# Performance work log

Measured on AMD Instinct MI355X. Metric: run time of the kernel, lower is better.

Reference implementation:

```python
import jax, jax.numpy as jnp
import numpy as np

D_MODEL = 1024
NUM_HEADS = 16
HEAD_SIZE = D_MODEL // NUM_HEADS
ROPE_BASE = 10000.0
RMS_EPS = 1e-6


def rms_norm(x, scale):
    # torchtune RMSNorm: fp32 compute, eps=1e-6, learned scale
    xf = x.astype(jnp.float32)
    n = xf * jax.lax.rsqrt(jnp.mean(xf * xf, axis=-1, keepdims=True) + RMS_EPS)
    return (n * scale).astype(x.dtype)


def rope(x):
    # torchtune RotaryPositionalEmbeddings: interleaved pairs. x: [B,T,H,hd]
    B, T, H, hd = x.shape
    half = hd // 2
    theta = 1.0 / (ROPE_BASE ** (jnp.arange(0, hd, 2, dtype=jnp.float32) / hd))  # [half]
    ang = jnp.arange(T, dtype=jnp.float32)[:, None] * theta[None, :]  # [T,half]
    cos = jnp.cos(ang)[None, :, None, :]  # [1,T,1,half]
    sin = jnp.sin(ang)[None, :, None, :]
    xs = x.reshape(B, T, H, half, 2)
    x0, x1 = xs[..., 0], xs[..., 1]
    out = jnp.stack([x0 * cos - x1 * sin, x1 * cos + x0 * sin], axis=-1)
    return out.reshape(B, T, H, hd).astype(x.dtype)


def setup_inputs() -> dict:
    key = jax.random.key(0)
    ks = jax.random.split(key, 10)
    s = 0.02
    D = D_MODEL
    return {
        "x": jax.random.normal(ks[0], (2, 2048, D), dtype=jnp.float32),
        "rms_scale": jnp.ones((D,), dtype=jnp.float32),
        "in_proj_w": jax.random.normal(ks[1], (3 * D, D), dtype=jnp.float32) * s,
        "in_proj_b": jnp.zeros((3 * D,), dtype=jnp.float32),
        "out_proj_w": jax.random.normal(ks[2], (D, D), dtype=jnp.float32) * s,
        "out_proj_b": jnp.zeros((D,), dtype=jnp.float32),
        "w1": jax.random.normal(ks[3], (4 * D, D), dtype=jnp.float32) * s,
        "b1": jnp.zeros((4 * D,), dtype=jnp.float32),
        "w2": jax.random.normal(ks[4], (D, 4 * D), dtype=jnp.float32) * s,
        "b2": jnp.zeros((D,), dtype=jnp.float32),
    }


def reference(x, rms_scale, in_proj_w, in_proj_b, out_proj_w, out_proj_b, w1, b1, w2, b2):
    B, T, D = x.shape
    H, hd = NUM_HEADS, HEAD_SIZE

    xn = rms_norm(x, rms_scale)
    # RoPE on pre-projection q/k (as in original module), value = xn
    q_in = rope(xn.reshape(B, T, H, hd)).reshape(B, T, D)
    k_in = rope(xn.reshape(B, T, H, hd)).reshape(B, T, D)
    v_in = xn

    Wq, Wk, Wv = jnp.split(in_proj_w, 3, axis=0)
    bq, bk, bv = jnp.split(in_proj_b, 3, axis=0)
    q = (q_in @ Wq.T + bq).reshape(B, T, H, hd).transpose(0, 2, 1, 3)  # [B,H,T,hd]
    k = (k_in @ Wk.T + bk).reshape(B, T, H, hd).transpose(0, 2, 1, 3)
    v = (v_in @ Wv.T + bv).reshape(B, T, H, hd).transpose(0, 2, 1, 3)

    scores = jnp.einsum('bhqd,bhkd->bhqk', q, k) / jnp.sqrt(jnp.float32(hd))
    causal = jnp.tril(jnp.ones((T, T), dtype=bool))  # True = keep
    scores = jnp.where(causal[None, None], scores, jnp.float32(-1e30))
    attn = jax.nn.softmax(scores, axis=-1)
    ctx = jnp.einsum('bhqk,bhkd->bhqd', attn, v)  # [B,H,T,hd]
    attn_out = ctx.transpose(0, 2, 1, 3).reshape(B, T, D) @ out_proj_w.T + out_proj_b

    # NOTE: original overwrites x with attention output (no residual on attention)
    y = attn_out
    yn = rms_norm(y, rms_scale)
    ffn = jax.nn.silu(yn @ w1.T + b1) @ w2.T + b2
    return y + ffn
```

## Files before the change

### kernel.cpp

```cpp
#include <hip/hip_runtime.h>
#include <math.h>
#include <stdint.h>

#define D_MODEL 1024
#define NUM_HEADS 16
#define HEAD_SIZE 64
#define SEQ_T 2048

typedef __bf16 bf16;
typedef __bf16 bf16x8 __attribute__((ext_vector_type(8)));
typedef float f32x4 __attribute__((ext_vector_type(4)));

__device__ __forceinline__ void gld_lds16(const bf16* g, bf16* l) {
    __builtin_amdgcn_global_load_lds(
        (__attribute__((address_space(1))) void*)(const_cast<bf16*>(g)),
        (__attribute__((address_space(3))) void*)(l), 16, 0, 0);
}

struct __align__(8) b4pack { bf16 v[4]; };

__global__ __launch_bounds__(256) void cast_all_weights(const float* __restrict__ s0, bf16* __restrict__ d0, int n0,
                                                        const float* __restrict__ s1, bf16* __restrict__ d1, int n1,
                                                        const float* __restrict__ s2, bf16* __restrict__ d2, int n2,
                                                        const float* __restrict__ s3, bf16* __restrict__ d3, int n3) {
    int i = (blockIdx.x * 256 + threadIdx.x) * 4;
    const float* src;
    bf16* dst;
    if (i < n0) { src = s0; dst = d0; }
    else if (i < n0 + n1) { i -= n0; src = s1; dst = d1; }
    else if (i < n0 + n1 + n2) { i -= n0 + n1; src = s2; dst = d2; }
    else { i -= n0 + n1 + n2; if (i >= n3) return; src = s3; dst = d3; }
    float4 v = *(const float4*)(src + i);
    b4pack o;
    o.v[0] = (bf16)v.x; o.v[1] = (bf16)v.y; o.v[2] = (bf16)v.z; o.v[3] = (bf16)v.w;
    *(b4pack*)(dst + i) = o;
}

__global__ __launch_bounds__(256) void rmsnorm_rope_kernel(const float* __restrict__ x,
                                                           const float* __restrict__ scale,
                                                           bf16* __restrict__ xn,
                                                           bf16* __restrict__ rp, int T) {
    __shared__ float red[4];
    int row = blockIdx.x;
    int t = row % T;
    const float* xp = x + (size_t)row * D_MODEL;
    int tid = threadIdx.x;
    float4 xv = *(const float4*)(xp + tid * 4);
    float s = xv.x * xv.x + xv.y * xv.y + xv.z * xv.z + xv.w * xv.w;
    for (int off = 32; off; off >>= 1) s += __shfl_down(s, off);
    if ((tid & 63) == 0) red[tid >> 6] = s;
    __syncthreads();
    if (tid == 0) red[0] = red[0] + red[1] + red[2] + red[3];
    __syncthreads();
    float inv = rsqrtf(red[0] * (1.0f / D_MODEL) + 1e-6f);
    float4 sc = *(const float4*)(scale + tid * 4);
    float n0 = xv.x * inv * sc.x, n1 = xv.y * inv * sc.y;
    float n2 = xv.z * inv * sc.z, n3 = xv.w * inv * sc.w;
    b4pack pn;
    pn.v[0] = (bf16)n0; pn.v[1] = (bf16)n1; pn.v[2] = (bf16)n2; pn.v[3] = (bf16)n3;
    *(b4pack*)(xn + (size_t)row * D_MODEL + tid * 4) = pn;
    int p0 = 2 * tid;
    float th0 = expf(-0.2878231366242557f * (float)(p0 & 31));
    float th1 = expf(-0.2878231366242557f * (float)((p0 + 1) & 31));
    float s0, c0, s1, c1;
    sincosf((float)t * th0, &s0, &c0);
    sincosf((float)t * th1, &s1, &c1);
    b4pack pr;
    pr.v[0] = (bf16)(n0 * c0 - n1 * s0);
    pr.v[1] = (bf16)(n1 * c0 + n0 * s0);
    pr.v[2] = (bf16)(n2 * c1 - n3 * s1);
    pr.v[3] = (bf16)(n3 * c1 + n2 * s1);
    *(b4pack*)(rp + (size_t)row * D_MODEL + tid * 4) = pr;
}

__global__ __launch_bounds__(256) void rmsnorm_kernel(const float* __restrict__ x,
                                                      const float* __restrict__ scale,
                                                      bf16* __restrict__ out) {
    __shared__ float red[4];
    int row = blockIdx.x;
    const float* xp = x + (size_t)row * D_MODEL;
    bf16* op = out + (size_t)row * D_MODEL;
    int tid = threadIdx.x;
    float s = 0.f;
    for (int i = tid; i < D_MODEL; i += 256) { float v = xp[i]; s += v * v; }
    for (int off = 32; off; off >>= 1) s += __shfl_down(s, off);
    if ((tid & 63) == 0) red[tid >> 6] = s;
    __syncthreads();
    if (tid == 0) red[0] = red[0] + red[1] + red[2] + red[3];
    __syncthreads();
    float inv = rsqrtf(red[0] * (1.0f / D_MODEL) + 1e-6f);
    for (int i = tid; i < D_MODEL; i += 256) op[i] = (bf16)(xp[i] * inv * scale[i]);
}

template <int ACT, int ADD, int OUT_BF16, int VT>
__global__ __launch_bounds__(256) void gemm_bf16(const bf16* __restrict__ A,
                                                 const bf16* __restrict__ A2, int splitN,
                                                 const bf16* __restrict__ W,
                                                 const float* __restrict__ bias,
                                                 float* __restrict__ Cf,
                                                 bf16* __restrict__ Cb,
                                                 bf16* __restrict__ Vtp, int Tlen,
                                                 int M, int N, int K) {
    __shared__ __align__(16) bf16 As[2][128 * 64];
    __shared__ __align__(16) bf16 Bs[2][128 * 64];
    int tid = threadIdx.x;
    int m0 = blockIdx.y * 128, n0 = blockIdx.x * 128;
    const bf16* Ag = (n0 < splitN) ? A : A2;

    int lane = tid & 63, w = tid >> 6;
    int wm = w >> 1, wn = w & 1;
    int lm = lane & 15, quad = lane >> 4;
    int lm7 = lm & 7;

    f32x4 acc[4][4];
#pragma unroll
    for (int i = 0; i < 4; i++)
#pragma unroll
        for (int j = 0; j < 4; j++)
#pragma unroll
            for (int r = 0; r < 4; r++) acc[i][j][r] = 0.f;

    int nt = K >> 6;

#pragma unroll
    for (int i = 0; i < 4; i++) {
        int cch = tid + 256 * i;
        int r = cch >> 3, cc = (cch & 7) ^ (r & 7);
        gld_lds16(Ag + (size_t)(m0 + r) * K + cc * 8, &As[0][0] + cch * 8);
        gld_lds16(W  + (size_t)(n0 + r) * K + cc * 8, &Bs[0][0] + cch * 8);
    }

    for (int t = 0; t < nt; ++t) {
        int cur = t & 1;
        if (t + 1 < nt) {
            int k0 = (t + 1) << 6;
            bf16* as = &As[cur ^ 1][0];
            bf16* bs = &Bs[cur ^ 1][0];
#pragma unroll
            for (int i = 0; i < 4; i++) {
                int cch = tid + 256 * i;
                int r = cch >> 3, cc = (cch & 7) ^ (r & 7);
                gld_lds16(Ag + (size_t)(m0 + r) * K + k0 + cc * 8, as + cch * 8);
                gld_lds16(W  + (size_t)(n0 + r) * K + k0 + cc * 8, bs + cch * 8);
            }
            asm volatile("s_waitcnt vmcnt(8)" ::: "memory");
        } else {
            asm volatile("s_waitcnt vmcnt(0)" ::: "memory");
        }
        __builtin_amdgcn_s_barrier();

        const bf16* as = &As[cur][0];
        const bf16* bs = &Bs[cur][0];
        bf16x8 af[4][2], bfr[4][2];
#pragma unroll
        for (int i = 0; i < 4; i++) {
            int row = wm * 64 + i * 16 + lm;
#pragma unroll
            for (int h2 = 0; h2 < 2; h2++)
                af[i][h2] = *(const bf16x8*)&as[row * 64 + ((h2 * 4 + quad) ^ lm7) * 8];
        }
#pragma unroll
        for (int j = 0; j < 4; j++) {
            int row = wn * 64 + j * 16 + lm;
#pragma unroll
            for (int h2 = 0; h2 < 2; h2++)
                bfr[j][h2] = *(const bf16x8*)&bs[row * 64 + ((h2 * 4 + quad) ^ lm7) * 8];
        }
#pragma unroll
        for (int i = 0; i < 4; i++)
#pragma unroll
            for (int j = 0; j < 4; j++) {
                acc[i][j] = __builtin_amdgcn_mfma_f32_16x16x32_bf16(af[i][0], bfr[j][0], acc[i][j], 0, 0, 0);
                acc[i][j] = __builtin_amdgcn_mfma_f32_16x16x32_bf16(af[i][1], bfr[j][1], acc[i][j], 0, 0, 0);
            }
        asm volatile("" ::: "memory");
        __builtin_amdgcn_s_barrier();
    }

    if (VT && n0 >= 2 * D_MODEL) {
#pragma unroll
        for (int j = 0; j < 4; j++) {
            int col = n0 + wn * 64 + j * 16 + lm;
            int dimg = col - 2 * D_MODEL;
            float bv = bias[col];
#pragma unroll
            for (int i = 0; i < 4; i++) {
                int row0 = m0 + wm * 64 + i * 16 + quad * 4;
                int bb = row0 / Tlen, t0 = row0 % Tlen;
                b4pack pk;
#pragma unroll
                for (int r = 0; r < 4; r++) pk.v[r] = (bf16)(acc[i][j][r] + bv);
                *(b4pack*)(Vtp + ((size_t)bb * D_MODEL + dimg) * Tlen + t0) = pk;
            }
        }
        return;
    }

#pragma unroll
    for (int j = 0; j < 4; j++) {
        int col = n0 + wn * 64 + j * 16 + lm;
        float bv = bias[col];
#pragma unroll
        for (int i = 0; i < 4; i++) {
#pragma unroll
            for (int r = 0; r < 4; r++) {
                int row = m0 + wm * 64 + i * 16 + quad * 4 + r;
                float v = acc[i][j][r] + bv;
                if (ACT == 1) v = v / (1.f + __expf(-v));
                size_t idx = (size_t)row * N + col;
                if (ADD) v += Cf[idx];
                if (OUT_BF16) Cb[idx] = (bf16)v;
                else Cf[idx] = v;
            }
        }
    }
}

template <int ADD>
__global__ __launch_bounds__(256) void gemm_bf16_skinny2(const bf16* __restrict__ A,
                                                         const bf16* __restrict__ W,
                                                         const float* __restrict__ bias,
                                                         float* __restrict__ Cf,
                                                         int M, int N, int K) {
    __shared__ __align__(16) bf16 As[2][64 * 64];
    __shared__ __align__(16) bf16 Bs[2][128 * 64];
    int tid = threadIdx.x;

    int nblk = gridDim.x;
    int q = nblk >> 3;
    int swz = (blockIdx.x & 7) * q + (blockIdx.x >> 3);
    int nb = swz & 7;
    int mb = swz >> 3;
    int m0 = mb * 64, n0 = nb * 128;

    int lane = tid & 63, w = tid >> 6;
    int wm = w >> 1, wn = w & 1;
    int lm = lane & 15, quad = lane >> 4;
    int lm7 = lm & 7;

    int ar0 = tid >> 3, ac0 = (tid & 7) ^ (ar0 & 7);
    int t1 = tid + 256;
    int ar1 = t1 >> 3, ac1 = (t1 & 7) ^ (ar1 & 7);

    f32x4 acc[2][4];
#pragma unroll
    for (int i = 0; i < 2; i++)
#pragma unroll
        for (int j = 0; j < 4; j++)
#pragma unroll
            for (int r = 0; r < 4; r++) acc[i][j][r] = 0.f;

    int nt = K >> 6;

    {
        gld_lds16(A + (size_t)(m0 + ar0) * K + ac0 * 8, &As[0][0] + tid * 8);
        gld_lds16(A + (size_t)(m0 + ar1) * K + ac1 * 8, &As[0][0] + t1 * 8);
#pragma unroll
        for (int i = 0; i < 4; i++) {
            int c = tid + 256 * i;
            int r = c >> 3, cc = (c & 7) ^ (r & 7);
            gld_lds16(W + (size_t)(n0 + r) * K + cc * 8, &Bs[0][0] + c * 8);
        }
    }

    for (int t = 0; t < nt; ++t) {
        int cur = t & 1;
        if (t + 1 < nt) {
            int k0 = (t + 1) << 6;
            bf16* as = &As[cur ^ 1][0];
            bf16* bs = &Bs[cur ^ 1][0];
            gld_lds16(A + (size_t)(m0 + ar0) * K + k0 + ac0 * 8, as + tid * 8);
            gld_lds16(A + (size_t)(m0 + ar1) * K + k0 + ac1 * 8, as + t1 * 8);
#pragma unroll
            for (int i = 0; i < 4; i++) {
                int c = tid + 256 * i;
                int r = c >> 3, cc = (c & 7) ^ (r & 7);
                gld_lds16(W + (size_t)(n0 + r) * K + k0 + cc * 8, bs + c * 8);
            }
            asm volatile("s_waitcnt vmcnt(6)" ::: "memory");
        } else {
            asm volatile("s_waitcnt vmcnt(0)" ::: "memory");
        }
        __builtin_amdgcn_s_barrier();

        const bf16* as = &As[cur][0];
        const bf16* bs = &Bs[cur][0];
        bf16x8 af[2][2], bfr[4][2];
#pragma unroll
        for (int i = 0; i < 2; i++) {
            int row = wm * 32 + i * 16 + lm;
#pragma unroll
            for (int h = 0; h < 2; h++)
                af[i][h] = *(const bf16x8*)&as[row * 64 + ((h * 4 + quad) ^ lm7) * 8];
        }
#pragma unroll
        for (int j = 0; j < 4; j++) {
            int row = wn * 64 + j * 16 + lm;
#pragma unroll
            for (int h = 0; h < 2; h++)
                bfr[j][h] = *(const bf16x8*)&bs[row * 64 + ((h * 4 + quad) ^ lm7) * 8];
        }
#pragma unroll
        for (int i = 0; i < 2; i++)
#pragma unroll
            for (int j = 0; j < 4; j++) {
                acc[i][j] = __builtin_amdgcn_mfma_f32_16x16x32_bf16(af[i][0], bfr[j][0], acc[i][j], 0, 0, 0);
                acc[i][j] = __builtin_amdgcn_mfma_f32_16x16x32_bf16(af[i][1], bfr[j][1], acc[i][j], 0, 0, 0);
            }
        asm volatile("" ::: "memory");
        __builtin_amdgcn_s_barrier();
    }

#pragma unroll
    for (int j = 0; j < 4; j++) {
        int col = n0 + wn * 64 + j * 16 + lm;
        float bv = bias[col];
#pragma unroll
        for (int i = 0; i < 2; i++) {
#pragma unroll
            for (int r = 0; r < 4; r++) {
                int row = m0 + wm * 32 + i * 16 + quad * 4 + r;
                float v = acc[i][j][r] + bv;
                size_t idx = (size_t)row * N + col;
                if (ADD) v += Cf[idx];
                Cf[idx] = v;
            }
        }
    }
}

__global__ __launch_bounds__(256, 2) void attn_mfma_kernel(const bf16* __restrict__ QKV,
                                                           const bf16* __restrict__ Vt,
                                                           bf16* __restrict__ Og, int T) {
    __shared__ __align__(16) bf16 Ks[2][2][64 * 64];
    __shared__ __align__(16) bf16 Vs[2][2][64 * 64];
    __shared__ __align__(16) bf16 Ps[4 * 16 * 64];
    const int ldq = 3 * D_MODEL;
    int bidx = blockIdx.x;
    int c = bidx & 7;
    int rest = bidx >> 3;
    int p = rest & 15;
    int bhoct = rest >> 4;
    int bh = bhoct * 8 + c;
    int qtA = 31 - p, qtB = p;
    int h = bh & (NUM_HEADS - 1), b = bh / NUM_HEADS;
    int tid = threadIdx.x;
    int w = tid >> 6, lane = tid & 63;
    int lm = lane & 15, quad = lane >> 4;
    int qrowA = qtA * 64 + w * 16, qrowB = qtB * 64 + w * 16;

    int s0 = tid, s1 = tid + 256;
    int sr0 = s0 >> 3, sc0 = (s0 & 7) ^ (sr0 & 7);
    int sr1 = s1 >> 3, sc1 = (s1 & 7) ^ (sr1 & 7);

    const bf16* QpA = QKV + ((size_t)(b * T + qrowA + lm)) * ldq + h * HEAD_SIZE + quad * 8;
    bf16x8 qfA0 = *(const bf16x8*)QpA;
    bf16x8 qfA1 = *(const bf16x8*)(QpA + 32);
    const bf16* QpB = QKV + ((size_t)(b * T + qrowB + lm)) * ldq + h * HEAD_SIZE + quad * 8;
    bf16x8 qfB0 = *(const bf16x8*)QpB;
    bf16x8 qfB1 = *(const bf16x8*)(QpB + 32);

    const bf16* Kbase = QKV + ((size_t)b * T) * ldq + D_MODEL + h * HEAD_SIZE;
    const bf16* Vbase = Vt + ((size_t)b * D_MODEL + h * HEAD_SIZE) * T;
    const float C = 0.1803368801111204f;
    bf16* PsW = Ps + w * 16 * 64;
    int lm7 = lm & 7;

    bf16x8 ones;
#pragma unroll
    for (int i = 0; i < 8; i++) ones[i] = (bf16)1.0f;

    f32x4 oA[4], oB[4], laccA, laccB;
#pragma unroll
    for (int r = 0; r < 4; r++) {
        oA[r] = (f32x4){0.f, 0.f, 0.f, 0.f};
        oB[r] = (f32x4){0.f, 0.f, 0.f, 0.f};
        laccA[r] = 0.f; laccB[r] = 0.f;
    }

    int nktA = (qtA + 2) >> 1;
    int nktB = (qtB + 2) >> 1;

    auto stage = [&](int buf, int k0) {
        gld_lds16(Kbase + (size_t)(k0 + sr0) * ldq + sc0 * 8, &Ks[buf][0][0] + s0 * 8);
        gld_lds16(Kbase + (size_t)(k0 + sr1) * ldq + sc1 * 8, &Ks[buf][0][0] + s1 * 8);
        gld_lds16(Kbase + (size_t)(k0 + 64 + sr0) * ldq + sc0 * 8, &Ks[buf][1][0] + s0 * 8);
        gld_lds16(Kbase + (size_t)(k0 + 64 + sr1) * ldq + sc1 * 8, &Ks[buf][1][0] + s1 * 8);
        gld_lds16(Vbase + (size_t)sr0 * T + k0 + sc0 * 8, &Vs[buf][0][0] + s0 * 8);
        gld_lds16(Vbase + (size_t)sr1 * T + k0 + sc1 * 8, &Vs[buf][0][0] + s1 * 8);
        gld_lds16(Vbase + (size_t)sr0 * T + k0 + 64 + sc0 * 8, &Vs[buf][1][0] + s0 * 8);
        gld_lds16(Vbase + (size_t)sr1 * T + k0 + 64 + sc1 * 8, &Vs[buf][1][0] + s1 * 8);
    };

    auto run_tile = [&](int cur, int k0, bf16x8 qf0, bf16x8 qf1, int qrow0,
                        f32x4 (&o)[4], f32x4& lacc, bool lastmask) {
        f32x4 sa[2][4];
        __builtin_amdgcn_s_setprio(1);
#pragma unroll
        for (int u = 0; u < 2; u++) {
            const bf16* Ksu = &Ks[cur][u][0];
#pragma unroll
            for (int jb = 0; jb < 4; jb++) {
                int n = jb * 16 + lm;
                bf16x8 kf0 = *(const bf16x8*)&Ksu[(n * 8 + (quad ^ lm7)) * 8];
                bf16x8 kf1 = *(const bf16x8*)&Ksu[(n * 8 + ((quad + 4) ^ lm7)) * 8];
                f32x4 a = {0.f, 0.f, 0.f, 0.f};
                a = __builtin_amdgcn_mfma_f32_16x16x32_bf16(qf0, kf0, a, 0, 0, 0);
                a = __builtin_amdgcn_mfma_f32_16x16x32_bf16(qf1, kf1, a, 0, 0, 0);
                sa[u][jb] = a;
            }
        }
        __builtin_amdgcn_s_setprio(0);
        if (lastmask) {
#pragma unroll
            for (int u = 0; u < 2; u++)
#pragma unroll
                for (int jb = 0; jb < 4; jb++)
#pragma unroll
                    for (int r = 0; r < 4; r++)
                        if (k0 + u * 64 + jb * 16 + lm > qrow0 + quad * 4 + r)
                            sa[u][jb][r] = -3.0e38f;
        }
#pragma unroll
        for (int u = 0; u < 2; u++) {
            const bf16* Vsu = &Vs[cur][u][0];
#pragma unroll
            for (int jb = 0; jb < 4; jb++) {
                int g = jb * 2 + (lm >> 3);
#pragma unroll
                for (int r = 0; r < 4; r++) {
                    int row = quad * 4 + r;
                    float pv = exp2f(sa[u][jb][r] * C);
                    PsW[row * 64 + ((g ^ (row & 7)) * 8) + lm7] = (bf16)pv;
                }
            }
            bf16x8 pf0 = *(const bf16x8*)&PsW[lm * 64 + ((quad ^ lm7) * 8)];
            bf16x8 pf1 = *(const bf16x8*)&PsW[lm * 64 + (((quad + 4) ^ lm7) * 8)];
            __builtin_amdgcn_s_setprio(1);
#pragma unroll
            for (int db = 0; db < 4; db++) {
                int n = db * 16 + lm;
                bf16x8 vf0 = *(const bf16x8*)&Vsu[(n * 8 + (quad ^ lm7)) * 8];
                bf16x8 vf1 = *(const bf16x8*)&Vsu[(n * 8 + ((quad + 4) ^ lm7)) * 8];
                o[db] = __builtin_amdgcn_mfma_f32_16x16x32_bf16(pf0, vf0, o[db], 0, 0, 0);
                o[db] = __builtin_amdgcn_mfma_f32_16x16x32_bf16(pf1, vf1, o[db], 0, 0, 0);
            }
            lacc = __builtin_amdgcn_mfma_f32_16x16x32_bf16(pf0, ones, lacc, 0, 0, 0);
            lacc = __builtin_amdgcn_mfma_f32_16x16x32_bf16(pf1, ones, lacc, 0, 0, 0);
            __builtin_amdgcn_s_setprio(0);
        }
    };

    stage(0, 0);
    for (int kt = 0; kt < nktA; kt++) {
        int cur = kt & 1;
        if (kt + 1 < nktA) {
            stage(cur ^ 1, (kt + 1) * 128);
            asm volatile("s_waitcnt vmcnt(8)" ::: "memory");
        } else {
            asm volatile("s_waitcnt vmcnt(0)" ::: "memory");
        }
        __builtin_amdgcn_s_barrier();
        asm volatile("" ::: "memory");
        int k0 = kt * 128;
        run_tile(cur, k0, qfA0, qfA1, qrowA, oA, laccA, kt == nktA - 1);
        if (kt < nktB)
            run_tile(cur, k0, qfB0, qfB1, qrowB, oB, laccB, kt == nktB - 1);
        asm volatile("" ::: "memory");
        __builtin_amdgcn_s_barrier();
    }

    {
        float inv[4];
#pragma unroll
        for (int r = 0; r < 4; r++) inv[r] = 1.f / laccA[r];
        bf16* Ob = Og + ((size_t)(b * T + qrowA + quad * 4)) * D_MODEL + h * HEAD_SIZE + lm;
#pragma unroll
        for (int r = 0; r < 4; r++)
#pragma unroll
            for (int db = 0; db < 4; db++)
                Ob[(size_t)r * D_MODEL + db * 16] = (bf16)(oA[db][r] * inv[r]);
    }
    {
        float inv[4];
#pragma unroll
        for (int r = 0; r < 4; r++) inv[r] = 1.f / laccB[r];
        bf16* Ob = Og + ((size_t)(b * T + qrowB + quad * 4)) * D_MODEL + h * HEAD_SIZE + lm;
#pragma unroll
        for (int r = 0; r < 4; r++)
#pragma unroll
            for (int db = 0; db < 4; db++)
                Ob[(size_t)r * D_MODEL + db * 16] = (bf16)(oB[db][r] * inv[r]);
    }
}

extern "C" void kernel_launch(void* const* d_in, const int* in_sizes, int n_in,
                              void* d_out, int out_size, void* d_ws, size_t ws_size,
                              hipStream_t stream) {
    const float* x          = (const float*)d_in[0];
    const float* rms_scale  = (const float*)d_in[1];
    const float* in_proj_w  = (const float*)d_in[2];
    const float* in_proj_b  = (const float*)d_in[3];
    const float* out_proj_w = (const float*)d_in[4];
    const float* out_proj_b = (const float*)d_in[5];
    const float* w1         = (const float*)d_in[6];
    const float* b1         = (const float*)d_in[7];
    const float* w2         = (const float*)d_in[8];
    const float* b2         = (const float*)d_in[9];
    float* out = (float*)d_out;

    const int rows = in_sizes[0] / D_MODEL;
    const int T = SEQ_T;
    const int B = rows / T;
    const int D = D_MODEL;

    bf16* inwb  = (bf16*)d_ws;
    bf16* outwb = inwb + (size_t)3 * D * D;
    bf16* w1b   = outwb + (size_t)D * D;
    bf16* w2b   = w1b + (size_t)4 * D * D;
    bf16* XNb   = w2b + (size_t)4 * D * D;
    bf16* RPb   = XNb + (size_t)rows * D;
    bf16* QKV   = RPb + (size_t)rows * D;
    bf16* Vt    = QKV + (size_t)rows * 3 * D;
    bf16* CTXb  = XNb;
    bf16* YNb   = RPb;
    bf16* H1b   = QKV;

    {
        int n0 = 3 * D * D, n1 = D * D, n2 = 4 * D * D, n3 = 4 * D * D;
        int tot4 = (n0 + n1 + n2 + n3) / 4;
        cast_all_weights<<<(tot4 + 255) / 256, 256, 0, stream>>>(
            in_proj_w, inwb, n0, out_proj_w, outwb, n1, w1, w1b, n2, w2, w2b, n3);
    }
    rmsnorm_rope_kernel<<<rows, 256, 0, stream>>>(x, rms_scale, XNb, RPb, T);
    {
        dim3 g(3 * D / 128, rows / 128);
        gemm_bf16<0, 0, 1, 1><<<g, 256, 0, stream>>>(RPb, XNb, 2 * D, inwb, in_proj_b,
                                                     nullptr, QKV, Vt, T, rows, 3 * D, D);
    }
    attn_mfma_kernel<<<B * NUM_HEADS * (T / 128), 256, 0, stream>>>(QKV, Vt, CTXb, T);
    {
        int nblk = (D / 128) * (rows / 64);
        gemm_bf16_skinny2<0><<<nblk, 256, 0, stream>>>(CTXb, outwb, out_proj_b, out,
                                                       rows, D, D);
    }
    rmsnorm_kernel<<<rows, 256, 0, stream>>>(out, rms_scale, YNb);
    {
        dim3 g(4 * D / 128, rows / 128);
        gemm_bf16<1, 0, 1, 0><<<g, 256, 0, stream>>>(YNb, YNb, 4 * D, w1b, b1,
                                                     nullptr, H1b, nullptr, 1, rows, 4 * D, D);
    }
    {
        int nblk = (D / 128) * (rows / 64);
        gemm_bf16_skinny2<1><<<nblk, 256, 0, stream>>>(H1b, w2b, b2, out,
                                                       rows, D, 4 * D);
    }
}
```

Before: 332.8 us.

## Split-K the skinny output GEMMs with atomic accumulation and bias prefill

The two N=1024 GEMMs (out-projection and FFN down-projection) now split K in two and accumulate partial tiles into the fp32 output with atomic adds, which doubles the block count. The output buffer is pre-filled with the out-projection bias inside the weight-cast kernel, so the first GEMM adds only partial sums. The second GEMM adds b2 from its first split on top of the existing output. This is meant to raise occupancy on a grid that launched too few blocks for the CU count. In exchange it adds atomic traffic, an extra full write of the output, and a float summation order that is no longer deterministic.

```diff
diff --git a/kernel.cpp b/kernel.cpp
--- a/kernel.cpp
+++ b/kernel.cpp
@@ -22,14 +22,22 @@
 __global__ __launch_bounds__(256) void cast_all_weights(const float* __restrict__ s0, bf16* __restrict__ d0, int n0,
                                                         const float* __restrict__ s1, bf16* __restrict__ d1, int n1,
                                                         const float* __restrict__ s2, bf16* __restrict__ d2, int n2,
-                                                        const float* __restrict__ s3, bf16* __restrict__ d3, int n3) {
+                                                        const float* __restrict__ s3, bf16* __restrict__ d3, int n3,
+                                                        const float* __restrict__ bsrc, float* __restrict__ bdst, int n4) {
     int i = (blockIdx.x * 256 + threadIdx.x) * 4;
     const float* src;
     bf16* dst;
     if (i < n0) { src = s0; dst = d0; }
     else if (i < n0 + n1) { i -= n0; src = s1; dst = d1; }
     else if (i < n0 + n1 + n2) { i -= n0 + n1; src = s2; dst = d2; }
-    else { i -= n0 + n1 + n2; if (i >= n3) return; src = s3; dst = d3; }
+    else if (i < n0 + n1 + n2 + n3) { i -= n0 + n1 + n2; src = s3; dst = d3; }
+    else {
+        i -= n0 + n1 + n2 + n3;
+        if (i >= n4) return;
+        float4 b = *(const float4*)(bsrc + (i & (D_MODEL - 1)));
+        *(float4*)(bdst + i) = b;
+        return;
+    }
     float4 v = *(const float4*)(src + i);
     b4pack o;
     o.v[0] = (bf16)v.x; o.v[1] = (bf16)v.y; o.v[2] = (bf16)v.z; o.v[3] = (bf16)v.w;
@@ -216,12 +224,12 @@
     }
 }
 
-template <int ADD>
-__global__ __launch_bounds__(256) void gemm_bf16_skinny2(const bf16* __restrict__ A,
-                                                         const bf16* __restrict__ W,
-                                                         const float* __restrict__ bias,
-                                                         float* __restrict__ Cf,
-                                                         int M, int N, int K) {
+template <int BIAS0, int SPLIT>
+__global__ __launch_bounds__(256) void gemm_bf16_skinny_sk(const bf16* __restrict__ A,
+                                                           const bf16* __restrict__ W,
+                                                           const float* __restrict__ bias,
+                                                           float* __restrict__ Cf,
+                                                           int M, int N, int K) {
     __shared__ __align__(16) bf16 As[2][64 * 64];
     __shared__ __align__(16) bf16 Bs[2][128 * 64];
     int tid = threadIdx.x;
@@ -230,8 +238,13 @@
     int q = nblk >> 3;
     int swz = (blockIdx.x & 7) * q + (blockIdx.x >> 3);
     int nb = swz & 7;
-    int mb = swz >> 3;
+    int rem = swz >> 3;
+    int mblocks = M >> 6;
+    int mb = rem % mblocks;
+    int sp = rem / mblocks;
     int m0 = mb * 64, n0 = nb * 128;
+    int kc = K / SPLIT;
+    int kbeg = sp * kc;
 
     int lane = tid & 63, w = tid >> 6;
     int wm = w >> 1, wn = w & 1;
@@ -250,23 +263,23 @@
 #pragma unroll
             for (int r = 0; r < 4; r++) acc[i][j][r] = 0.f;
 
-    int nt = K >> 6;
-
-    {
-        gld_lds16(A + (size_t)(m0 + ar0) * K + ac0 * 8, &As[0][0] + tid * 8);
-        gld_lds16(A + (size_t)(m0 + ar1) * K + ac1 * 8, &As[0][0] + t1 * 8);
+    int nt = kc >> 6;
+
+    {
+        gld_lds16(A + (size_t)(m0 + ar0) * K + kbeg + ac0 * 8, &As[0][0] + tid * 8);
+        gld_lds16(A + (size_t)(m0 + ar1) * K + kbeg + ac1 * 8, &As[0][0] + t1 * 8);
 #pragma unroll
         for (int i = 0; i < 4; i++) {
             int c = tid + 256 * i;
             int r = c >> 3, cc = (c & 7) ^ (r & 7);
-            gld_lds16(W + (size_t)(n0 + r) * K + cc * 8, &Bs[0][0] + c * 8);
+            gld_lds16(W + (size_t)(n0 + r) * K + kbeg + cc * 8, &Bs[0][0] + c * 8);
         }
     }
 
     for (int t = 0; t < nt; ++t) {
         int cur = t & 1;
         if (t + 1 < nt) {
-            int k0 = (t + 1) << 6;
+            int k0 = kbeg + ((t + 1) << 6);
             bf16* as = &As[cur ^ 1][0];
             bf16* bs = &Bs[cur ^ 1][0];
             gld_lds16(A + (size_t)(m0 + ar0) * K + k0 + ac0 * 8, as + tid * 8);
@@ -314,16 +327,13 @@
 #pragma unroll
     for (int j = 0; j < 4; j++) {
         int col = n0 + wn * 64 + j * 16 + lm;
-        float bv = bias[col];
+        float bv = (BIAS0 && sp == 0) ? bias[col] : 0.f;
 #pragma unroll
         for (int i = 0; i < 2; i++) {
 #pragma unroll
             for (int r = 0; r < 4; r++) {
                 int row = m0 + wm * 32 + i * 16 + quad * 4 + r;
-                float v = acc[i][j][r] + bv;
-                size_t idx = (size_t)row * N + col;
-                if (ADD) v += Cf[idx];
-                Cf[idx] = v;
+                unsafeAtomicAdd(Cf + (size_t)row * N + col, acc[i][j][r] + bv);
             }
         }
     }
@@ -528,9 +538,11 @@
 
     {
         int n0 = 3 * D * D, n1 = D * D, n2 = 4 * D * D, n3 = 4 * D * D;
-        int tot4 = (n0 + n1 + n2 + n3) / 4;
+        int n4 = rows * D;
+        int tot4 = (n0 + n1 + n2 + n3 + n4) / 4;
         cast_all_weights<<<(tot4 + 255) / 256, 256, 0, stream>>>(
-            in_proj_w, inwb, n0, out_proj_w, outwb, n1, w1, w1b, n2, w2, w2b, n3);
+            in_proj_w, inwb, n0, out_proj_w, outwb, n1, w1, w1b, n2, w2, w2b, n3,
+            out_proj_b, out, n4);
     }
     rmsnorm_rope_kernel<<<rows, 256, 0, stream>>>(x, rms_scale, XNb, RPb, T);
     {
@@ -540,9 +552,9 @@
     }
     attn_mfma_kernel<<<B * NUM_HEADS * (T / 128), 256, 0, stream>>>(QKV, Vt, CTXb, T);
     {
-        int nblk = (D / 128) * (rows / 64);
-        gemm_bf16_skinny2<0><<<nblk, 256, 0, stream>>>(CTXb, outwb, out_proj_b, out,
-                                                       rows, D, D);
+        int nblk = 2 * (rows / 64) * (D / 128);
+        gemm_bf16_skinny_sk<0, 2><<<nblk, 256, 0, stream>>>(CTXb, outwb, out_proj_b,
+                                                            out, rows, D, D);
     }
     rmsnorm_kernel<<<rows, 256, 0, stream>>>(out, rms_scale, YNb);
     {
@@ -551,8 +563,8 @@
                                                      nullptr, H1b, nullptr, 1, rows, 4 * D, D);
     }
     {
-        int nblk = (D / 128) * (rows / 64);
-        gemm_bf16_skinny2<1><<<nblk, 256, 0, stream>>>(H1b, w2b, b2, out,
-                                                       rows, D, 4 * D);
-    }
-}
+        int nblk = 2 * (rows / 64) * (D / 128);
+        gemm_bf16_skinny_sk<1, 2><<<nblk, 256, 0, stream>>>(H1b, w2b, b2,
+                                                            out, rows, D, 4 * D);
+    }
+}
```

New measurement: 366.0 us. 10.0% more time.

## Use split-K 128x128 GEMM with atomic accumulation for FFN down-projection

Applied to the files above, without the earlier changes.

Replaces the 64x128-tile skinny kernel for the w2 GEMM (K=4096) with a 128x128-tile kernel that splits K in two and atomically adds partial results into the output, which already holds the attention output for the residual. Larger tiles raise data reuse per block, and split-K keeps the grid at 512 blocks. The cost is float atomic traffic to the output and a non-deterministic summation order.

```diff
diff --git a/kernel.cpp b/kernel.cpp
--- a/kernel.cpp
+++ b/kernel.cpp
@@ -216,6 +216,114 @@
     }
 }
 
+template <int SPLIT>
+__global__ __launch_bounds__(256) void gemm128_sk(const bf16* __restrict__ A,
+                                                  const bf16* __restrict__ W,
+                                                  const float* __restrict__ bias,
+                                                  float* __restrict__ Cf,
+                                                  int M, int N, int K) {
+    __shared__ __align__(16) bf16 As[2][128 * 64];
+    __shared__ __align__(16) bf16 Bs[2][128 * 64];
+    int tid = threadIdx.x;
+
+    int nblk = gridDim.x;
+    int q = nblk >> 3;
+    int swz = (blockIdx.x & 7) * q + (blockIdx.x >> 3);
+    int nnb = N >> 7;
+    int nb = swz % nnb;
+    int rem = swz / nnb;
+    int mblocks = M >> 7;
+    int mb = rem % mblocks;
+    int sp = rem / mblocks;
+    int m0 = mb * 128, n0 = nb * 128;
+    int kc = K / SPLIT;
+    int kbeg = sp * kc;
+
+    int lane = tid & 63, w = tid >> 6;
+    int wm = w >> 1, wn = w & 1;
+    int lm = lane & 15, quad = lane >> 4;
+    int lm7 = lm & 7;
+
+    f32x4 acc[4][4];
+#pragma unroll
+    for (int i = 0; i < 4; i++)
+#pragma unroll
+        for (int j = 0; j < 4; j++)
+#pragma unroll
+            for (int r = 0; r < 4; r++) acc[i][j][r] = 0.f;
+
+    int nt = kc >> 6;
+
+#pragma unroll
+    for (int i = 0; i < 4; i++) {
+        int cch = tid + 256 * i;
+        int r = cch >> 3, cc = (cch & 7) ^ (r & 7);
+        gld_lds16(A + (size_t)(m0 + r) * K + kbeg + cc * 8, &As[0][0] + cch * 8);
+        gld_lds16(W + (size_t)(n0 + r) * K + kbeg + cc * 8, &Bs[0][0] + cch * 8);
+    }
+
+    for (int t = 0; t < nt; ++t) {
+        int cur = t & 1;
+        if (t + 1 < nt) {
+            int k0 = kbeg + ((t + 1) << 6);
+            bf16* as = &As[cur ^ 1][0];
+            bf16* bs = &Bs[cur ^ 1][0];
+#pragma unroll
+            for (int i = 0; i < 4; i++) {
+                int cch = tid + 256 * i;
+                int r = cch >> 3, cc = (cch & 7) ^ (r & 7);
+                gld_lds16(A + (size_t)(m0 + r) * K + k0 + cc * 8, as + cch * 8);
+                gld_lds16(W + (size_t)(n0 + r) * K + k0 + cc * 8, bs + cch * 8);
+            }
+            asm volatile("s_waitcnt vmcnt(8)" ::: "memory");
+        } else {
+            asm volatile("s_waitcnt vmcnt(0)" ::: "memory");
+        }
+        __builtin_amdgcn_s_barrier();
+
+        const bf16* as = &As[cur][0];
+        const bf16* bs = &Bs[cur][0];
+        bf16x8 af[4][2], bfr[4][2];
+#pragma unroll
+        for (int i = 0; i < 4; i++) {
+            int row = wm * 64 + i * 16 + lm;
+#pragma unroll
+            for (int h2 = 0; h2 < 2; h2++)
+                af[i][h2] = *(const bf16x8*)&as[row * 64 + ((h2 * 4 + quad) ^ lm7) * 8];
+        }
+#pragma unroll
+        for (int j = 0; j < 4; j++) {
+            int row = wn * 64 + j * 16 + lm;
+#pragma unroll
+            for (int h2 = 0; h2 < 2; h2++)
+                bfr[j][h2] = *(const bf16x8*)&bs[row * 64 + ((h2 * 4 + quad) ^ lm7) * 8];
+        }
+#pragma unroll
+        for (int i = 0; i < 4; i++)
+#pragma unroll
+            for (int j = 0; j < 4; j++) {
+                acc[i][j] = __builtin_amdgcn_mfma_f32_16x16x32_bf16(af[i][0], bfr[j][0], acc[i][j], 0, 0, 0);
+                acc[i][j] = __builtin_amdgcn_mfma_f32_16x16x32_bf16(af[i][1], bfr[j][1], acc[i][j], 0, 0, 0);
+            }
+        asm volatile("" ::: "memory");
+        __builtin_amdgcn_s_barrier();
+    }
+
+#pragma unroll
+    for (int j = 0; j < 4; j++) {
+        int col = n0 + wn * 64 + j * 16 + lm;
+        float bv = (sp == 0) ? bias[col] : 0.f;
+#pragma unroll
+        for (int i = 0; i < 4; i++) {
+#pragma unroll
+            for (int r = 0; r < 4; r++) {
+                int row = m0 + wm * 64 + i * 16 + quad * 4 + r;
+                unsafeAtomicAdd(Cf + (size_t)row * N + col, acc[i][j][r] + bv);
+            }
+        }
+    }
+}
+
 template <int ADD>
 __global__ __launch_bounds__(256) void gemm_bf16_skinny2(const bf16* __restrict__ A,
                                                          const bf16* __restrict__ W,
@@ -551,8 +659,7 @@
                                                      nullptr, H1b, nullptr, 1, rows, 4 * D, D);
     }
     {
-        int nblk = (D / 128) * (rows / 64);
-        gemm_bf16_skinny2<1><<<nblk, 256, 0, stream>>>(H1b, w2b, b2, out,
-                                                       rows, D, 4 * D);
-    }
-}
+        int nblk = 2 * (rows / 128) * (D / 128);
+        gemm128_sk<2><<<nblk, 256, 0, stream>>>(H1b, w2b, b2, out, rows, D, 4 * D);
+    }
+}
```

Result: no change. 327.1 us (-1.7%).
